# Performance work log

Measured on AMD Instinct MI355X. Metric: run time of the kernel, lower is better.

Reference implementation:

```python
import jax, jax.numpy as jnp
import numpy as np

N = 50000
E = 1600000
D_CONTENT, D_STYLE, D_CAT = 768, 128, 32  # concat feature = 2*D_CAT = 64
H1, H2, NCLS = 64, 64, 2


def _lin_params(key, din, dout, bias=True):
    k1, k2 = jax.random.split(key)
    s = 1.0 / np.sqrt(din)
    W = jax.random.uniform(k1, (din, dout), jnp.float32, -s, s)
    b = jax.random.uniform(k2, (dout,), jnp.float32, -s, s) if bias else None
    return W, b


def setup_inputs() -> dict:
    key = jax.random.key(0)
    ks = jax.random.split(key, 16)
    x_content = jax.random.normal(ks[0], (N, D_CONTENT), jnp.float32)
    x_style = jax.random.normal(ks[1], (N, D_STYLE), jnp.float32)
    edge_index = jax.random.randint(ks[2], (2, E), 0, N, jnp.int64)
    edge_type = jax.random.randint(ks[3], (E,), 0, 4, jnp.int64)
    Wp, bp = _lin_params(ks[4], D_CONTENT, D_CAT)
    Ws, bs = _lin_params(ks[5], D_STYLE, D_CAT)
    # SAGEConv: lin_l (aggregated neighbors, has bias), lin_r (root, no bias)
    Wl1, bl1 = _lin_params(ks[6], 2 * D_CAT, H1)
    Wr1, _ = _lin_params(ks[7], 2 * D_CAT, H1, bias=False)
    Wl2, bl2 = _lin_params(ks[8], H1, H2)
    Wr2, _ = _lin_params(ks[9], H1, H2, bias=False)
    Wl3, bl3 = _lin_params(ks[10], H2, H2)
    Wr3, _ = _lin_params(ks[11], H2, H2, bias=False)
    Wo, bo = _lin_params(ks[12], H2, NCLS)
    return dict(x_content=x_content, x_style=x_style, edge_index=edge_index,
                edge_type=edge_type, Wp=Wp, bp=bp, Ws=Ws, bs=bs,
                Wl1=Wl1, bl1=bl1, Wr1=Wr1, Wl2=Wl2, bl2=bl2, Wr2=Wr2,
                Wl3=Wl3, bl3=bl3, Wr3=Wr3, Wo=Wo, bo=bo)


def _sage_conv(x, src, dst, Wl, bl, Wr):
    # mean aggregation of source-node features at destination nodes
    msg_sum = jax.ops.segment_sum(x[src], dst, num_segments=N)  # [N, d]
    deg = jax.ops.segment_sum(jnp.ones((src.shape[0],), x.dtype), dst,
                              num_segments=N)
    agg = msg_sum / jnp.maximum(deg, 1.0)[:, None]
    return agg @ Wl + bl + x @ Wr


def reference(x_content, x_style, edge_index, edge_type,
              Wp, bp, Ws, bs, Wl1, bl1, Wr1, Wl2, bl2, Wr2,
              Wl3, bl3, Wr3, Wo, bo):
    src, dst = edge_index[0], edge_index[1]
    x = jnp.concatenate([x_content @ Wp + bp, x_style @ Ws + bs], axis=1)
    x = jax.nn.relu(_sage_conv(x, src, dst, Wl1, bl1, Wr1))  # dropout = id (eval)
    x = jax.nn.relu(_sage_conv(x, src, dst, Wl2, bl2, Wr2))
    x = jax.nn.relu(_sage_conv(x, src, dst, Wl3, bl3, Wr3))
    return x @ Wo + bo
```

## Files before the change

kernel.cpp:

```cpp
#include <hip/hip_runtime.h>
#include <stdint.h>


typedef __attribute__((ext_vector_type(8))) unsigned short u16x8;
typedef __attribute__((ext_vector_type(4))) float f32x4;

static __device__ __forceinline__ float bf2f(unsigned short u) {
  union { unsigned int i; float f; } v;
  v.i = ((unsigned int)u) << 16;
  return v.f;
}

static __device__ __forceinline__ unsigned short f2bf(float f) {
  union { float f; unsigned int i; } v;
  v.f = f;
  unsigned int u = v.i;
  unsigned int r = (u + 0x7FFFu + ((u >> 16) & 1u)) >> 16;
  return (unsigned short)r;
}

template <bool BF>
static __device__ __forceinline__ float ldf(const void* p, long long i) {
  if (BF) return bf2f(((const unsigned short*)p)[i]);
  return ((const float*)p)[i];
}

template <bool BF>
static __device__ __forceinline__ void load8(const void* p, long long idx,
                                             float* out) {
  if (BF) {
    u16x8 v = *(const u16x8*)((const unsigned short*)p + idx);
#pragma unroll
    for (int j = 0; j < 8; ++j) out[j] = bf2f(v[j]);
  } else {
    f32x4 a = *(const f32x4*)((const float*)p + idx);
    f32x4 b = *(const f32x4*)((const float*)p + idx + 4);
#pragma unroll
    for (int j = 0; j < 4; ++j) {
      out[j] = a[j];
      out[4 + j] = b[j];
    }
  }
}

template <bool BF>
static __device__ __forceinline__ void loadw8q(const void* p, int row, int q,
                                               float* wv) {
  if (BF) {
    const unsigned int* d = (const unsigned int*)p + row * 16 + q * 4;
#pragma unroll
    for (int t = 0; t < 4; ++t) {
      unsigned int u = d[t];
      union { unsigned int i; float f; } c0, c1;
      c0.i = u << 16;
      c1.i = u & 0xFFFF0000u;
      wv[2 * t + 0] = c0.f;
      wv[2 * t + 1] = c1.f;
    }
  } else {
    const float* d = (const float*)p + row * 32 + q * 8;
#pragma unroll
    for (int t = 0; t < 8; ++t) wv[t] = d[t];
  }
}

static __device__ __forceinline__ int clampN(int v, int N) {
  return v < 0 ? 0 : (v >= N ? N - 1 : v);
}

__global__ void k_detect(const void* Wp, const int* ei, int* flags) {
  if (threadIdx.x == 0 && blockIdx.x == 0) {
    const unsigned short* w = (const unsigned short*)Wp;
    int bf = 1;
    for (int i = 0; i < 64; ++i) {
      float v = fabsf(bf2f(w[i]));
      if (!(v < 1.0f)) bf = 0;
    }
    flags[0] = bf;
    int i64 = 1;
    for (int i = 0; i < 32; ++i)
      if (ei[2 * i + 1] != 0) i64 = 0;
    flags[1] = i64;
  }
}

static __device__ __forceinline__ int edge_src(const int* ei, int e, int E,
                                               int i64) {
  return i64 ? ei[2 * (long long)e] : ei[e];
}
static __device__ __forceinline__ int edge_dst(const int* ei, int e, int E,
                                               int i64) {
  return i64 ? ei[2 * ((long long)E + e)] : ei[(long long)E + e];
}


__global__ __launch_bounds__(256) void k_deg(const int* __restrict__ ei, int E,
                                             int N, int* __restrict__ cnt,
                                             const int* __restrict__ flags) {
  int e = blockIdx.x * 256 + threadIdx.x;
  if (e < E) {
    int d = clampN(edge_dst(ei, e, E, flags[1]), N);
    atomicAdd(&cnt[d], 1);
  }
}

__global__ __launch_bounds__(256) void k_scan1(const int* __restrict__ cnt,
                                               int* __restrict__ rowptr,
                                               int* __restrict__ bsum, int N) {
  __shared__ int sh[256];
  int t = threadIdx.x;
  int base = blockIdx.x * 1024 + t * 4;
  int v0 = 0, v1 = 0, v2 = 0, v3 = 0;
  if (base + 0 < N) v0 = cnt[base + 0];
  if (base + 1 < N) v1 = cnt[base + 1];
  if (base + 2 < N) v2 = cnt[base + 2];
  if (base + 3 < N) v3 = cnt[base + 3];
  int s = v0 + v1 + v2 + v3;
  sh[t] = s;
  __syncthreads();
  int acc = s;
  for (int off = 1; off < 256; off <<= 1) {
    int x = 0;
    if (t >= off) x = sh[t - off];
    __syncthreads();
    acc += x;
    sh[t] = acc;
    __syncthreads();
  }
  int run = acc - s;
  if (base + 0 < N) rowptr[base + 0] = run;
  run += v0;
  if (base + 1 < N) rowptr[base + 1] = run;
  run += v1;
  if (base + 2 < N) rowptr[base + 2] = run;
  run += v2;
  if (base + 3 < N) rowptr[base + 3] = run;
  run += v3;
  if (t == 255) bsum[blockIdx.x] = acc;
}

__global__ void k_scan2(int* __restrict__ bsum, int nb,
                        int* __restrict__ rowptr, int N) {
  if (threadIdx.x == 0 && blockIdx.x == 0) {
    int run = 0;
    for (int i = 0; i < nb; ++i) {
      int v = bsum[i];
      bsum[i] = run;
      run += v;
    }
    rowptr[N] = run;
  }
}

__global__ __launch_bounds__(256) void k_scan3(int* __restrict__ rowptr,
                                               int* __restrict__ cursor,
                                               const int* __restrict__ bsum,
                                               int N) {
  int i = blockIdx.x * 256 + threadIdx.x;
  if (i < N) {
    int v = rowptr[i] + bsum[i >> 10];
    rowptr[i] = v;
    cursor[i] = v;
  }
}

__global__ __launch_bounds__(256) void k_scatter(const int* __restrict__ ei,
                                                 int E, int N,
                                                 int* __restrict__ cursor,
                                                 int* __restrict__ colbuf,
                                                 const int* __restrict__ flags) {
  int e = blockIdx.x * 256 + threadIdx.x;
  if (e < E) {
    int i64 = flags[1];
    int s = clampN(edge_src(ei, e, E, i64), N);
    int d = clampN(edge_dst(ei, e, E, i64), N);
    int p = atomicAdd(&cursor[d], 1);
    if (p >= 0 && p < E) colbuf[p] = s;
  }
}

template <bool BF>
static __device__ void project_body(const void* __restrict__ xc,
                                    const void* __restrict__ xs,
                                    const void* __restrict__ Wp,
                                    const void* __restrict__ bp,
                                    const void* __restrict__ Ws,
                                    const void* __restrict__ bs,
                                    float* __restrict__ h0, int N,
                                    float* __restrict__ red) {
  int tid = (int)threadIdx.x;
  int w = __builtin_amdgcn_readfirstlane(tid >> 6);
  int q = w & 3;
  int h = w >> 2;
  int lane = tid & 63;
  int node = (int)blockIdx.x * 64 + lane;
  int nclamp = node < N ? node : (N - 1);

  float accc[8], accs[8];
#pragma unroll
  for (int r = 0; r < 8; ++r) {
    accc[r] = 0.f;
    accs[r] = 0.f;
  }

  {
    long long xoff = (long long)nclamp * 768 + h * 384;
    int rbase = h * 384;
    float a0[8], a1[8], n0[8], n1[8];
    load8<BF>(xc, xoff + 0, a0);
    load8<BF>(xc, xoff + 8, a1);
#pragma unroll 1
    for (int k = 0; k < 384; k += 16) {
      int k2 = (k + 16 < 384) ? (k + 16) : 0;
      load8<BF>(xc, xoff + k2, n0);
      load8<BF>(xc, xoff + k2 + 8, n1);
#pragma unroll
      for (int j = 0; j < 8; ++j) {
        float wv[8];
        loadw8q<BF>(Wp, rbase + k + j, q, wv);
#pragma unroll
        for (int r = 0; r < 8; ++r) accc[r] += a0[j] * wv[r];
      }
#pragma unroll
      for (int j = 0; j < 8; ++j) {
        float wv[8];
        loadw8q<BF>(Wp, rbase + k + 8 + j, q, wv);
#pragma unroll
        for (int r = 0; r < 8; ++r) accc[r] += a1[j] * wv[r];
      }
#pragma unroll
      for (int j = 0; j < 8; ++j) {
        a0[j] = n0[j];
        a1[j] = n1[j];
      }
    }
  }

  {
    long long soff = (long long)nclamp * 128 + h * 64;
    int rbase = h * 64;
    float a0[8], a1[8], n0[8], n1[8];
    load8<BF>(xs, soff + 0, a0);
    load8<BF>(xs, soff + 8, a1);
#pragma unroll 1
    for (int k = 0; k < 64; k += 16) {
      int k2 = (k + 16 < 64) ? (k + 16) : 0;
      load8<BF>(xs, soff + k2, n0);
      load8<BF>(xs, soff + k2 + 8, n1);
#pragma unroll
      for (int j = 0; j < 8; ++j) {
        float wv[8];
        loadw8q<BF>(Ws, rbase + k + j, q, wv);
#pragma unroll
        for (int r = 0; r < 8; ++r) accs[r] += a0[j] * wv[r];
      }
#pragma unroll
      for (int j = 0; j < 8; ++j) {
        float wv[8];
        loadw8q<BF>(Ws, rbase + k + 8 + j, q, wv);
#pragma unroll
        for (int r = 0; r < 8; ++r) accs[r] += a1[j] * wv[r];
      }
#pragma unroll
      for (int j = 0; j < 8; ++j) {
        a0[j] = n0[j];
        a1[j] = n1[j];
      }
    }
  }

  {
    float* row = red + (h * 64 + lane) * 65;
#pragma unroll
    for (int r = 0; r < 8; ++r) {
      row[8 * q + r] = accc[r];
      row[32 + 8 * q + r] = accs[r];
    }
  }
  __syncthreads();

  {
    int n2 = tid >> 3;
    int oc = (tid & 7) * 8;
    int gnode = (int)blockIdx.x * 64 + n2;
    if (gnode < N) {
      float v[8];
#pragma unroll
      for (int i = 0; i < 8; ++i) {
        int out = oc + i;
        float b = (out < 32) ? ldf<BF>(bp, out) : ldf<BF>(bs, out - 32);
        v[i] = red[n2 * 65 + out] + red[(64 + n2) * 65 + out] + b;
      }
      float* orow = h0 + (long long)gnode * 64 + oc;
      f32x4 v0 = {v[0], v[1], v[2], v[3]};
      f32x4 v1 = {v[4], v[5], v[6], v[7]};
      *(f32x4*)orow = v0;
      *(f32x4*)(orow + 4) = v1;
    }
  }
}

__global__ __launch_bounds__(512, 8) void k_project(
    const void* __restrict__ xc, const void* __restrict__ xs,
    const void* __restrict__ Wp, const void* __restrict__ bp,
    const void* __restrict__ Ws, const void* __restrict__ bs,
    float* __restrict__ h0, int N, const int* __restrict__ flags) {
  __shared__ float red[2 * 64 * 65];
  if (flags[0])
    project_body<true>(xc, xs, Wp, bp, Ws, bs, h0, N, red);
  else
    project_body<false>(xc, xs, Wp, bp, Ws, bs, h0, N, red);
}

template <bool BF>
static __device__ void layer_body(const float* __restrict__ hin,
                                  const int* __restrict__ rowptr,
                                  const int* __restrict__ colbuf,
                                  const void* Wl, const void* bl,
                                  const void* Wr, float* __restrict__ hout,
                                  int N, int last, const void* Wo,
                                  const void* bo, void* outp) {
  int node = (int)((blockIdx.x * blockDim.x + threadIdx.x) >> 6);
  int lane = (int)(threadIdx.x & 63);
  if (node >= N) return;
  int rs = rowptr[node], re = rowptr[node + 1];
  float xself = hin[(long long)node * 64 + lane];
  float agg0 = 0.f, agg1 = 0.f, agg2 = 0.f, agg3 = 0.f;
  float agg4 = 0.f, agg5 = 0.f, agg6 = 0.f, agg7 = 0.f;
  for (int cb = rs; cb < re; cb += 64) {
    int sidx = 0;
    if (cb + lane < re) sidx = clampN(colbuf[cb + lane], N);
    int c = re - cb;
    if (c > 64) c = 64;
    int t = 0;
    for (; t + 8 <= c; t += 8) {
      int s0 = __builtin_amdgcn_readlane(sidx, t + 0);
      int s1 = __builtin_amdgcn_readlane(sidx, t + 1);
      int s2 = __builtin_amdgcn_readlane(sidx, t + 2);
      int s3 = __builtin_amdgcn_readlane(sidx, t + 3);
      int s4 = __builtin_amdgcn_readlane(sidx, t + 4);
      int s5 = __builtin_amdgcn_readlane(sidx, t + 5);
      int s6 = __builtin_amdgcn_readlane(sidx, t + 6);
      int s7 = __builtin_amdgcn_readlane(sidx, t + 7);
      float v0 = hin[(long long)s0 * 64 + lane];
      float v1 = hin[(long long)s1 * 64 + lane];
      float v2 = hin[(long long)s2 * 64 + lane];
      float v3 = hin[(long long)s3 * 64 + lane];
      float v4 = hin[(long long)s4 * 64 + lane];
      float v5 = hin[(long long)s5 * 64 + lane];
      float v6 = hin[(long long)s6 * 64 + lane];
      float v7 = hin[(long long)s7 * 64 + lane];
      agg0 += v0;
      agg1 += v1;
      agg2 += v2;
      agg3 += v3;
      agg4 += v4;
      agg5 += v5;
      agg6 += v6;
      agg7 += v7;
    }
    for (; t < c; ++t) {
      int s = __builtin_amdgcn_readlane(sidx, t);
      agg0 += hin[(long long)s * 64 + lane];
    }
  }
  float agg = ((agg0 + agg1) + (agg2 + agg3)) + ((agg4 + agg5) + (agg6 + agg7));
  int deg = re - rs;
  if (deg > 0) agg *= (1.f / (float)deg);

  float o = ldf<BF>(bl, lane);
#pragma unroll 8
  for (int d = 0; d < 64; ++d) {
    float ad = __uint_as_float(
        __builtin_amdgcn_readlane(__float_as_uint(agg), d));
    float xd = __uint_as_float(
        __builtin_amdgcn_readlane(__float_as_uint(xself), d));
    o += ad * ldf<BF>(Wl, d * 64 + lane);
    o += xd * ldf<BF>(Wr, d * 64 + lane);
  }
  o = fmaxf(o, 0.f);

  if (!last) {
    hout[(long long)node * 64 + lane] = o;
  } else {
    float c0 = o * ldf<BF>(Wo, lane * 2 + 0);
    float c1 = o * ldf<BF>(Wo, lane * 2 + 1);
    for (int off = 32; off > 0; off >>= 1) {
      c0 += __shfl_xor(c0, off, 64);
      c1 += __shfl_xor(c1, off, 64);
    }
    if (lane == 0) {
      float r0 = c0 + ldf<BF>(bo, 0);
      float r1 = c1 + ldf<BF>(bo, 1);
      if (BF) {
        unsigned short* o16 = (unsigned short*)outp;
        o16[(long long)node * 2 + 0] = f2bf(r0);
        o16[(long long)node * 2 + 1] = f2bf(r1);
      } else {
        float* o32 = (float*)outp;
        o32[(long long)node * 2 + 0] = r0;
        o32[(long long)node * 2 + 1] = r1;
      }
    }
  }
}

__global__ __launch_bounds__(256) void k_layer(
    const float* hin, const int* rowptr, const int* colbuf, const void* Wl,
    const void* bl, const void* Wr, float* hout, int N, int last,
    const void* Wo, const void* bo, void* outp, const int* __restrict__ flags) {
  if (flags[0])
    layer_body<true>(hin, rowptr, colbuf, Wl, bl, Wr, hout, N, last, Wo, bo,
                     outp);
  else
    layer_body<false>(hin, rowptr, colbuf, Wl, bl, Wr, hout, N, last, Wo, bo,
                      outp);
}


extern "C" void kernel_launch(void* const* d_in, const int* in_sizes, int n_in,
                              void* d_out, int out_size, void* d_ws,
                              size_t ws_size, hipStream_t stream) {
  const void* xc = d_in[0];
  const void* xs = d_in[1];
  const int* ei = (const int*)d_in[2];
  const void* Wp = d_in[4];
  const void* bp = d_in[5];
  const void* Ws = d_in[6];
  const void* bs = d_in[7];
  const void* Wl1 = d_in[8];
  const void* bl1 = d_in[9];
  const void* Wr1 = d_in[10];
  const void* Wl2 = d_in[11];
  const void* bl2 = d_in[12];
  const void* Wr2 = d_in[13];
  const void* Wl3 = d_in[14];
  const void* bl3 = d_in[15];
  const void* Wr3 = d_in[16];
  const void* Wo = d_in[17];
  const void* bo = d_in[18];

  int N = out_size / 2;
  int E = in_sizes[3];

  char* ws = (char*)d_ws;
  size_t off = 0;
  auto alloc = [&](size_t bytes) {
    char* p = ws + off;
    off += (bytes + 255) & ~(size_t)255;
    return p;
  };
  int* colbuf = (int*)alloc((size_t)E * 4);
  int* cnt = (int*)alloc((size_t)N * 4);
  int* rowptr = (int*)alloc((size_t)(N + 1) * 4);
  int* cursor = (int*)alloc((size_t)N * 4);
  int* bsum = (int*)alloc(4096);
  int* flags = (int*)alloc(256);
  float* h0 = (float*)alloc((size_t)N * 64 * 4);
  float* h1 = (float*)alloc((size_t)N * 64 * 4);
  (void)ws_size;
  (void)n_in;

  k_detect<<<1, 64, 0, stream>>>(Wp, ei, flags);

  hipMemsetAsync(cnt, 0, (size_t)N * 4, stream);
  int eb = (E + 255) / 256;
  k_deg<<<eb, 256, 0, stream>>>(ei, E, N, cnt, flags);
  int sb = (N + 1023) / 1024;
  k_scan1<<<sb, 256, 0, stream>>>(cnt, rowptr, bsum, N);
  k_scan2<<<1, 64, 0, stream>>>(bsum, sb, rowptr, N);
  k_scan3<<<(N + 255) / 256, 256, 0, stream>>>(rowptr, cursor, bsum, N);
  k_scatter<<<eb, 256, 0, stream>>>(ei, E, N, cursor, colbuf, flags);

  int pb = (N + 63) / 64;
  k_project<<<pb, 512, 0, stream>>>(xc, xs, Wp, bp, Ws, bs, h0, N, flags);

  int nb4 = (N + 3) / 4;
  k_layer<<<nb4, 256, 0, stream>>>(h0, rowptr, colbuf, Wl1, bl1, Wr1, h1, N, 0,
                                   nullptr, nullptr, nullptr, flags);
  k_layer<<<nb4, 256, 0, stream>>>(h1, rowptr, colbuf, Wl2, bl2, Wr2, h0, N, 0,
                                   nullptr, nullptr, nullptr, flags);
  k_layer<<<nb4, 256, 0, stream>>>(h0, rowptr, colbuf, Wl3, bl3, Wr3, h1, N, 1,
                                   Wo, bo, d_out, flags);
}
```

Measured before the change: 826.7 us.

## Stage projection inputs through double-buffered LDS tiles with coalesced loads

The projection kernel now loads 64-column chunks of each node's content and style features cooperatively, with coalesced 16-element reads per thread, into a double-buffered shared-memory tile, prefetching the next chunk while the current one is consumed. Each of 4 waves computes 8 output columns over the full K range, which removes the earlier split-K reduction through shared memory and drops the block from 512 to 256 threads. Before, each lane read its own node row with strided per-lane loads. The change adds a barrier per chunk, and each wave now does more FMA work because the K range is no longer split across waves.

```diff
diff --git a/kernel.cpp b/kernel.cpp
--- a/kernel.cpp
+++ b/kernel.cpp
@@ -23,24 +23,6 @@
 static __device__ __forceinline__ float ldf(const void* p, long long i) {
   if (BF) return bf2f(((const unsigned short*)p)[i]);
   return ((const float*)p)[i];
-}
-
-template <bool BF>
-static __device__ __forceinline__ void load8(const void* p, long long idx,
-                                             float* out) {
-  if (BF) {
-    u16x8 v = *(const u16x8*)((const unsigned short*)p + idx);
-#pragma unroll
-    for (int j = 0; j < 8; ++j) out[j] = bf2f(v[j]);
-  } else {
-    f32x4 a = *(const f32x4*)((const float*)p + idx);
-    f32x4 b = *(const f32x4*)((const float*)p + idx + 4);
-#pragma unroll
-    for (int j = 0; j < 4; ++j) {
-      out[j] = a[j];
-      out[4 + j] = b[j];
-    }
-  }
 }
 
 template <bool BF>
@@ -187,129 +169,137 @@
                                     const void* __restrict__ Ws,
                                     const void* __restrict__ bs,
                                     float* __restrict__ h0, int N,
-                                    float* __restrict__ red) {
+                                    float* __restrict__ xt) {
   int tid = (int)threadIdx.x;
   int w = __builtin_amdgcn_readfirstlane(tid >> 6);
-  int q = w & 3;
-  int h = w >> 2;
   int lane = tid & 63;
   int node = (int)blockIdx.x * 64 + lane;
-  int nclamp = node < N ? node : (N - 1);
-
-  float accc[8], accs[8];
+
+  int sn = tid >> 2;
+  int sj = tid & 3;
+  int gsn = (int)blockIdx.x * 64 + sn;
+  int gsnc = gsn < N ? gsn : (N - 1);
+
+  float c[8], s[8];
 #pragma unroll
   for (int r = 0; r < 8; ++r) {
-    accc[r] = 0.f;
-    accs[r] = 0.f;
-  }
-
-  {
-    long long xoff = (long long)nclamp * 768 + h * 384;
-    int rbase = h * 384;
-    float a0[8], a1[8], n0[8], n1[8];
-    load8<BF>(xc, xoff + 0, a0);
-    load8<BF>(xc, xoff + 8, a1);
+    c[r] = 0.f;
+    s[r] = 0.f;
+  }
+
+  u16x8 pr0 = {}, pr1 = {};
+  f32x4 pf0 = {}, pf1 = {}, pf2 = {}, pf3 = {};
+
+  auto stage_load = [&](int t) {
+    long long idx;
+    const void* src;
+    if (t < 12) {
+      src = xc;
+      idx = (long long)gsnc * 768 + t * 64 + 16 * sj;
+    } else {
+      src = xs;
+      idx = (long long)gsnc * 128 + (t - 12) * 64 + 16 * sj;
+    }
+    if (BF) {
+      const unsigned short* p = (const unsigned short*)src + idx;
+      pr0 = *(const u16x8*)p;
+      pr1 = *(const u16x8*)(p + 8);
+    } else {
+      const float* p = (const float*)src + idx;
+      pf0 = *(const f32x4*)(p + 0);
+      pf1 = *(const f32x4*)(p + 4);
+      pf2 = *(const f32x4*)(p + 8);
+      pf3 = *(const f32x4*)(p + 12);
+    }
+  };
+
+  auto stage_write = [&](int t) {
+    float* row = xt + (t & 1) * (64 * 65) + sn * 65 + 16 * sj;
+    if (BF) {
+#pragma unroll
+      for (int i = 0; i < 8; ++i) row[i] = bf2f(pr0[i]);
+#pragma unroll
+      for (int i = 0; i < 8; ++i) row[8 + i] = bf2f(pr1[i]);
+    } else {
+#pragma unroll
+      for (int i = 0; i < 4; ++i) {
+        row[i] = pf0[i];
+        row[4 + i] = pf1[i];
+        row[8 + i] = pf2[i];
+        row[12 + i] = pf3[i];
+      }
+    }
+  };
+
+  stage_load(0);
+  stage_write(0);
+  __syncthreads();
+
 #pragma unroll 1
-    for (int k = 0; k < 384; k += 16) {
-      int k2 = (k + 16 < 384) ? (k + 16) : 0;
-      load8<BF>(xc, xoff + k2, n0);
-      load8<BF>(xc, xoff + k2 + 8, n1);
-#pragma unroll
-      for (int j = 0; j < 8; ++j) {
-        float wv[8];
-        loadw8q<BF>(Wp, rbase + k + j, q, wv);
-#pragma unroll
-        for (int r = 0; r < 8; ++r) accc[r] += a0[j] * wv[r];
+  for (int t = 0; t < 14; ++t) {
+    if (t + 1 < 14) stage_load(t + 1);
+
+    const float* xrow = xt + (t & 1) * (64 * 65) + lane * 65;
+    if (t < 12) {
+      int rbase = t * 64;
+#pragma unroll 1
+      for (int k0 = 0; k0 < 64; k0 += 8) {
+#pragma unroll
+        for (int kk = 0; kk < 8; ++kk) {
+          float xv = xrow[k0 + kk];
+          float wv[8];
+          loadw8q<BF>(Wp, rbase + k0 + kk, w, wv);
+#pragma unroll
+          for (int r = 0; r < 8; ++r) c[r] += xv * wv[r];
+        }
       }
-#pragma unroll
-      for (int j = 0; j < 8; ++j) {
-        float wv[8];
-        loadw8q<BF>(Wp, rbase + k + 8 + j, q, wv);
-#pragma unroll
-        for (int r = 0; r < 8; ++r) accc[r] += a1[j] * wv[r];
+    } else {
+      int rbase = (t - 12) * 64;
+#pragma unroll 1
+      for (int k0 = 0; k0 < 64; k0 += 8) {
+#pragma unroll
+        for (int kk = 0; kk < 8; ++kk) {
+          float xv = xrow[k0 + kk];
+          float wv[8];
+          loadw8q<BF>(Ws, rbase + k0 + kk, w, wv);
+#pragma unroll
+          for (int r = 0; r < 8; ++r) s[r] += xv * wv[r];
+        }
       }
-#pragma unroll
-      for (int j = 0; j < 8; ++j) {
-        a0[j] = n0[j];
-        a1[j] = n1[j];
-      }
-    }
-  }
-
-  {
-    long long soff = (long long)nclamp * 128 + h * 64;
-    int rbase = h * 64;
-    float a0[8], a1[8], n0[8], n1[8];
-    load8<BF>(xs, soff + 0, a0);
-    load8<BF>(xs, soff + 8, a1);
-#pragma unroll 1
-    for (int k = 0; k < 64; k += 16) {
-      int k2 = (k + 16 < 64) ? (k + 16) : 0;
-      load8<BF>(xs, soff + k2, n0);
-      load8<BF>(xs, soff + k2 + 8, n1);
-#pragma unroll
-      for (int j = 0; j < 8; ++j) {
-        float wv[8];
-        loadw8q<BF>(Ws, rbase + k + j, q, wv);
-#pragma unroll
-        for (int r = 0; r < 8; ++r) accs[r] += a0[j] * wv[r];
-      }
-#pragma unroll
-      for (int j = 0; j < 8; ++j) {
-        float wv[8];
-        loadw8q<BF>(Ws, rbase + k + 8 + j, q, wv);
-#pragma unroll
-        for (int r = 0; r < 8; ++r) accs[r] += a1[j] * wv[r];
-      }
-#pragma unroll
-      for (int j = 0; j < 8; ++j) {
-        a0[j] = n0[j];
-        a1[j] = n1[j];
-      }
-    }
-  }
-
-  {
-    float* row = red + (h * 64 + lane) * 65;
-#pragma unroll
-    for (int r = 0; r < 8; ++r) {
-      row[8 * q + r] = accc[r];
-      row[32 + 8 * q + r] = accs[r];
-    }
-  }
-  __syncthreads();
-
-  {
-    int n2 = tid >> 3;
-    int oc = (tid & 7) * 8;
-    int gnode = (int)blockIdx.x * 64 + n2;
-    if (gnode < N) {
-      float v[8];
-#pragma unroll
-      for (int i = 0; i < 8; ++i) {
-        int out = oc + i;
-        float b = (out < 32) ? ldf<BF>(bp, out) : ldf<BF>(bs, out - 32);
-        v[i] = red[n2 * 65 + out] + red[(64 + n2) * 65 + out] + b;
-      }
-      float* orow = h0 + (long long)gnode * 64 + oc;
-      f32x4 v0 = {v[0], v[1], v[2], v[3]};
-      f32x4 v1 = {v[4], v[5], v[6], v[7]};
-      *(f32x4*)orow = v0;
-      *(f32x4*)(orow + 4) = v1;
-    }
-  }
-}
-
-__global__ __launch_bounds__(512, 8) void k_project(
+    }
+
+    if (t + 1 < 14) stage_write(t + 1);
+    __syncthreads();
+  }
+
+  if (node < N) {
+    float* orow = h0 + (long long)node * 64;
+    f32x4 v;
+#pragma unroll
+    for (int r = 0; r < 4; ++r) v[r] = c[r] + ldf<BF>(bp, 8 * w + r);
+    *(f32x4*)(orow + 8 * w) = v;
+#pragma unroll
+    for (int r = 0; r < 4; ++r) v[r] = c[4 + r] + ldf<BF>(bp, 8 * w + 4 + r);
+    *(f32x4*)(orow + 8 * w + 4) = v;
+#pragma unroll
+    for (int r = 0; r < 4; ++r) v[r] = s[r] + ldf<BF>(bs, 8 * w + r);
+    *(f32x4*)(orow + 32 + 8 * w) = v;
+#pragma unroll
+    for (int r = 0; r < 4; ++r) v[r] = s[4 + r] + ldf<BF>(bs, 8 * w + 4 + r);
+    *(f32x4*)(orow + 32 + 8 * w + 4) = v;
+  }
+}
+
+__global__ __launch_bounds__(256) void k_project(
     const void* __restrict__ xc, const void* __restrict__ xs,
     const void* __restrict__ Wp, const void* __restrict__ bp,
     const void* __restrict__ Ws, const void* __restrict__ bs,
     float* __restrict__ h0, int N, const int* __restrict__ flags) {
-  __shared__ float red[2 * 64 * 65];
+  __shared__ float xt[2 * 64 * 65];
   if (flags[0])
-    project_body<true>(xc, xs, Wp, bp, Ws, bs, h0, N, red);
+    project_body<true>(xc, xs, Wp, bp, Ws, bs, h0, N, xt);
   else
-    project_body<false>(xc, xs, Wp, bp, Ws, bs, h0, N, red);
+    project_body<false>(xc, xs, Wp, bp, Ws, bs, h0, N, xt);
 }
 
 template <bool BF>
@@ -473,7 +463,7 @@
   k_scatter<<<eb, 256, 0, stream>>>(ei, E, N, cursor, colbuf, flags);
 
   int pb = (N + 63) / 64;
-  k_project<<<pb, 512, 0, stream>>>(xc, xs, Wp, bp, Ws, bs, h0, N, flags);
+  k_project<<<pb, 256, 0, stream>>>(xc, xs, Wp, bp, Ws, bs, h0, N, flags);
 
   int nb4 = (N + 3) / 4;
   k_layer<<<nb4, 256, 0, stream>>>(h0, rowptr, colbuf, Wl1, bl1, Wr1, h1, N, 0,
```

Measured after the change: 786.9 us. 4.8% less time.
